# Kernel optimization log

Measured on AMD Instinct MI355X. Metric: run time of the kernel, lower is better.

The kernel has to match this reference:

```python
import jax, jax.numpy as jnp
import numpy as np

DIM = 512
HEADS = 8
EPS = 1e-5


def layer_norm(x, g, b):
    mu = jnp.mean(x, axis=-1, keepdims=True)
    var = jnp.mean(jnp.square(x - mu), axis=-1, keepdims=True)
    return (x - mu) * jax.lax.rsqrt(var + EPS) * g + b


def setup_inputs() -> dict:
    key = jax.random.key(0)
    ks = jax.random.split(key, 8)
    d = DIM
    s = 0.02
    return {
        "x": jax.random.normal(ks[0], (2, d, 64, 64), jnp.float32),
        "ln1_g": jnp.ones((d,), jnp.float32),
        "ln1_b": jnp.zeros((d,), jnp.float32),
        "w_qkv": jax.random.normal(ks[1], (d, 3 * d), jnp.float32) * s,
        "b_qkv": jnp.zeros((3 * d,), jnp.float32),
        "w_proj": jax.random.normal(ks[2], (d, d), jnp.float32) * s,
        "b_proj": jnp.zeros((d,), jnp.float32),
        "ln2_g": jnp.ones((d,), jnp.float32),
        "ln2_b": jnp.zeros((d,), jnp.float32),
        "w_ffn1": jax.random.normal(ks[3], (d, 4 * d), jnp.float32) * s,
        "b_ffn1": jnp.zeros((4 * d,), jnp.float32),
        "w_ffn2": jax.random.normal(ks[4], (4 * d, d), jnp.float32) * s,
        "b_ffn2": jnp.zeros((d,), jnp.float32),
    }


def reference(x, ln1_g, ln1_b, w_qkv, b_qkv, w_proj, b_proj,
              ln2_g, ln2_b, w_ffn1, b_ffn1, w_ffn2, b_ffn2):
    B, C, H, W = x.shape
    hd = C // HEADS
    x_in = x
    t = x.reshape(B, C, H * W).transpose(0, 2, 1)  # [B, N, C]
    h = layer_norm(t, ln1_g, ln1_b)
    qkv = h @ w_qkv + b_qkv  # [B, N, 3C]
    q, k, v = jnp.split(qkv, 3, axis=-1)
    def to_heads(a):
        return a.reshape(B, -1, HEADS, hd).transpose(0, 2, 1, 3)  # [B, h, N, hd]
    q, k, v = to_heads(q), to_heads(k), to_heads(v)
    # NOTE: module scales by 1/sqrt(C), not 1/sqrt(head_dim)
    attn = jnp.einsum('bhqd,bhkd->bhqk', q, k) / jnp.sqrt(jnp.float32(C))
    attn = jax.nn.softmax(attn, axis=-1)
    out = jnp.einsum('bhqk,bhkd->bhqd', attn, v)
    out = out.transpose(0, 2, 1, 3).reshape(B, -1, C)
    out = out @ w_proj + b_proj
    t = t + out
    h2 = layer_norm(t, ln2_g, ln2_b)
    ffn = jax.nn.relu(h2 @ w_ffn1 + b_ffn1) @ w_ffn2 + b_ffn2
    t = t + ffn
    y = t.transpose(0, 2, 1).reshape(B, C, H, W)
    return y + x_in
```

## Files before the change

kernel.cpp:

```cpp
#include <hip/hip_runtime.h>
#include <hip/hip_bf16.h>

typedef __bf16 bf16;
typedef __bf16 bf16x8 __attribute__((ext_vector_type(8)));
typedef __bf16 bf16x4 __attribute__((ext_vector_type(4)));
typedef __bf16 bf16x2 __attribute__((ext_vector_type(2)));
typedef float f32x4 __attribute__((ext_vector_type(4)));
typedef int int4v __attribute__((ext_vector_type(4)));
typedef int int2v __attribute__((ext_vector_type(2)));

#define DEV static __device__ __forceinline__

DEV void gload16(const void* g, void* l) {
    __builtin_amdgcn_global_load_lds(
        (const __attribute__((address_space(1))) void*)g,
        (__attribute__((address_space(3))) void*)l, 16, 0, 0);
}

DEV f32x4 mfma16(bf16x8 a, bf16x8 b, f32x4 c) {
    return __builtin_amdgcn_mfma_f32_16x16x32_bf16(a, b, c, 0, 0, 0);
}

DEV int cvtpk(float lo, float hi) {
    int r;
    asm("v_cvt_pk_bf16_f32 %0, %1, %2" : "=v"(r) : "v"(lo), "v"(hi));
    return r;
}

DEV float rexp2(float x) {
    float r;
    asm("v_exp_f32 %0, %1" : "=v"(r) : "v"(x));
    return r;
}

__global__ __launch_bounds__(512, 2)
void k_pre(const float* __restrict__ x, const float* __restrict__ gg,
           const float* __restrict__ bb, bf16* __restrict__ h,
           const float* __restrict__ w0, const float* __restrict__ w1,
           const float* __restrict__ w2, const float* __restrict__ w3,
           bf16* __restrict__ d0, bf16* __restrict__ d1,
           bf16* __restrict__ d2, bf16* __restrict__ d3) {
    __shared__ char sm[35840];
    int bid = blockIdx.x;
    int t = threadIdx.x;

    if (bid >= 256) {
        float* tile = (float*)sm;
        int tt = bid - 256;
        const float* w;
        bf16* d;
        int K, N, ti;
        if (tt < 768)       { w = w0; d = d0; K = 512;  N = 1536; ti = tt; }
        else if (tt < 1024) { w = w1; d = d1; K = 512;  N = 512;  ti = tt - 768; }
        else if (tt < 2048) { w = w2; d = d2; K = 512;  N = 2048; ti = tt - 1024; }
        else                { w = w3; d = d3; K = 2048; N = 512;  ti = tt - 2048; }
        int ntn = N >> 5;
        int kt = ti / ntn, ntile = ti % ntn;
        int k0 = kt * 32, n0 = ntile * 32;
        int nl = t & 31, kl = t >> 5;
#pragma unroll
        for (int i = 0; i < 2; i++) {
            int k = kl + i * 16;
            tile[k * 33 + nl] = w[(size_t)(k0 + k) * N + n0 + nl];
        }
        __syncthreads();
        int kl2 = t & 31, nl2 = t >> 5;
#pragma unroll
        for (int i = 0; i < 2; i++) {
            int n = nl2 + i * 16;
            d[(size_t)(n0 + n) * K + k0 + kl2] = (bf16)tile[kl2 * 33 + n];
        }
        return;
    }

    bf16* big = (bf16*)sm;
    float* red = (float*)(sm + 33536);
    float* mures = (float*)(sm + 35584);
    int nt = bid & 127, b = bid >> 7;
    int n0 = nt * 32;

    int n = t & 31, cg = t >> 5;
    const float* xp = x + (size_t)b * 512 * 4096 +
                      (size_t)(cg * 32) * 4096 + n0 + n;
    float s = 0.f, ss = 0.f;
#pragma unroll
    for (int i = 0; i < 32; i++) {
        float v = xp[(size_t)i * 4096];
        s += v;
        ss += v * v;
        big[n * 524 + cg * 32 + i] = (bf16)v;
    }
    s += __shfl_xor(s, 32);
    ss += __shfl_xor(ss, 32);
    int w = t >> 6, l = t & 63;
    if (l < 32) {
        red[(w * 32 + n) * 2] = s;
        red[(w * 32 + n) * 2 + 1] = ss;
    }
    __syncthreads();
    if (t < 32) {
        float ts = 0.f, tss = 0.f;
#pragma unroll
        for (int ww = 0; ww < 8; ww++) {
            ts += red[(ww * 32 + t) * 2];
            tss += red[(ww * 32 + t) * 2 + 1];
        }
        float mu = ts * (1.f / 512.f);
        float var = tss * (1.f / 512.f) - mu * mu;
        mures[t * 2] = mu;
        mures[t * 2 + 1] = rsqrtf(var + 1e-5f);
    }
    __syncthreads();

    int nw = t >> 4, cs = t & 15;
    float mu = mures[nw * 2], rs = mures[nw * 2 + 1];
    bf16* hd = h + (size_t)(b * 4096 + n0 + nw) * 512;
#pragma unroll
    for (int j = 0; j < 4; j++) {
        int c = cs * 8 + j * 128;
        bf16x8 vv = *(const bf16x8*)&big[nw * 524 + c];
        f32x4 g0v = *(const f32x4*)(gg + c);
        f32x4 g1v = *(const f32x4*)(gg + c + 4);
        f32x4 b0v = *(const f32x4*)(bb + c);
        f32x4 b1v = *(const f32x4*)(bb + c + 4);
        bf16x8 o;
#pragma unroll
        for (int k = 0; k < 4; k++) {
            o[k] = (bf16)(((float)vv[k] - mu) * rs * g0v[k] + b0v[k]);
            o[k + 4] = (bf16)(((float)vv[k + 4] - mu) * rs * g1v[k] + b1v[k]);
        }
        *(bf16x8*)(hd + c) = o;
    }
}

__global__ __launch_bounds__(512, 2)
void k_tln2(const float* __restrict__ x, const bf16* __restrict__ po,
            const float* __restrict__ gg, const float* __restrict__ bb,
            bf16* __restrict__ h) {
    __shared__ char sm[69632];
    bf16* big = (bf16*)sm;
    float* red = (float*)(sm + 33536);
    float* mures = (float*)(sm + 35584);
    bf16* pob = (bf16*)(sm + 35840);

    int t = threadIdx.x;
    int bid = blockIdx.x;
    int nt = bid & 127, b = bid >> 7;
    int n0 = nt * 32;

    {
        int rr = t >> 4, cs16 = t & 15;
        const bf16* ps = po + (size_t)(b * 4096 + n0 + rr) * 512 + cs16 * 32;
#pragma unroll
        for (int j = 0; j < 4; j++)
            *(bf16x8*)&pob[rr * 524 + cs16 * 32 + j * 8] =
                *(const bf16x8*)(ps + j * 8);
        __syncthreads();
    }

    int n = t & 31, cg = t >> 5;
    const float* xp = x + (size_t)b * 512 * 4096 +
                      (size_t)(cg * 32) * 4096 + n0 + n;
    float s = 0.f, ss = 0.f;
#pragma unroll
    for (int i = 0; i < 32; i++) {
        float v = xp[(size_t)i * 4096] + (float)pob[n * 524 + cg * 32 + i];
        s += v;
        ss += v * v;
        big[n * 524 + cg * 32 + i] = (bf16)v;
    }
    s += __shfl_xor(s, 32);
    ss += __shfl_xor(ss, 32);
    int w = t >> 6, l = t & 63;
    if (l < 32) {
        red[(w * 32 + n) * 2] = s;
        red[(w * 32 + n) * 2 + 1] = ss;
    }
    __syncthreads();
    if (t < 32) {
        float ts = 0.f, tss = 0.f;
#pragma unroll
        for (int ww = 0; ww < 8; ww++) {
            ts += red[(ww * 32 + t) * 2];
            tss += red[(ww * 32 + t) * 2 + 1];
        }
        float mu = ts * (1.f / 512.f);
        float var = tss * (1.f / 512.f) - mu * mu;
        mures[t * 2] = mu;
        mures[t * 2 + 1] = rsqrtf(var + 1e-5f);
    }
    __syncthreads();

    int nw = t >> 4, cs = t & 15;
    float mu = mures[nw * 2], rs = mures[nw * 2 + 1];
    bf16* hd = h + (size_t)(b * 4096 + n0 + nw) * 512;
#pragma unroll
    for (int j = 0; j < 4; j++) {
        int c = cs * 8 + j * 128;
        bf16x8 vv = *(const bf16x8*)&big[nw * 524 + c];
        f32x4 g0v = *(const f32x4*)(gg + c);
        f32x4 g1v = *(const f32x4*)(gg + c + 4);
        f32x4 b0v = *(const f32x4*)(bb + c);
        f32x4 b1v = *(const f32x4*)(bb + c + 4);
        bf16x8 o;
#pragma unroll
        for (int k = 0; k < 4; k++) {
            o[k] = (bf16)(((float)vv[k] - mu) * rs * g0v[k] + b0v[k]);
            o[k + 4] = (bf16)(((float)vv[k + 4] - mu) * rs * g1v[k] + b1v[k]);
        }
        *(bf16x8*)(hd + c) = o;
    }
}

template <int MODE, int BN>
__global__ __launch_bounds__(256, BN == 64 ? 3 : 2)
void k_gemm(const bf16* __restrict__ A, const bf16* __restrict__ BT,
            const float* __restrict__ bias, bf16* __restrict__ outb,
            bf16* __restrict__ vtout, const float* __restrict__ xin,
            const bf16* __restrict__ poin, float* __restrict__ yout,
            int M, int N, int K) {
    constexpr int CG = BN / 32;
    constexpr int BSZ = CG * 4096;
    __shared__ char smem[32768 + 2 * BSZ];
    int ntn = N / BN;
    int nwg = gridDim.x;
    int bid = blockIdx.x;
    int cpx = nwg >> 3;
    bid = (bid & 7) * cpx + (bid >> 3);
    int bm = bid / ntn, bn = bid % ntn;
    int m0 = bm * 128, n0 = bn * BN;
    int tid = threadIdx.x;
    int w = tid >> 6, l = tid & 63;
    int wm = w >> 1, wn = w & 1;
    int l15 = l & 15, lg = l >> 4;

    f32x4 acc[4][CG];
#pragma unroll
    for (int i = 0; i < 4; i++)
#pragma unroll
        for (int j = 0; j < CG; j++) acc[i][j] = (f32x4){0.f, 0.f, 0.f, 0.f};

    int srow = tid >> 3, sphys = tid & 7;
    int lrow_a = wm * 64 + l15;
    int lrow_b = wn * (BN / 2) + l15;

#define GEMM_STAGE(k0v, bb)                                                  \
    do {                                                                     \
        _Pragma("unroll") for (int s = 0; s < 4; s++) {                      \
            int row = s * 32 + srow;                                         \
            int k16 = sphys ^ (row & 7);                                     \
            gload16(A + (size_t)(m0 + row) * K + (k0v) + k16 * 8,            \
                    smem + (bb) * 16384 + s * 4096 + tid * 16);              \
        }                                                                    \
        _Pragma("unroll") for (int s = 0; s < CG; s++) {                     \
            int row = s * 32 + srow;                                         \
            int k16 = sphys ^ (row & 7);                                     \
            gload16(BT + (size_t)(n0 + row) * K + (k0v) + k16 * 8,           \
                    smem + 32768 + (bb) * BSZ + s * 4096 + tid * 16);        \
        }                                                                    \
    } while (0)

    int nk = K >> 6;
    GEMM_STAGE(0, 0);
    int cur = 0;
    for (int kt = 0; kt < nk; kt++) {
        if (kt + 1 < nk) {
            GEMM_STAGE((kt + 1) << 6, cur ^ 1);
            if constexpr (BN == 128)
                asm volatile("s_waitcnt vmcnt(8)" ::: "memory");
            else
                asm volatile("s_waitcnt vmcnt(6)" ::: "memory");
        } else {
            asm volatile("s_waitcnt vmcnt(0)" ::: "memory");
        }
        __builtin_amdgcn_s_barrier();
        __builtin_amdgcn_sched_barrier(0);
        const char* pA = smem + cur * 16384;
        const char* pB = smem + 32768 + cur * BSZ;
#pragma unroll
        for (int ks = 0; ks < 2; ks++) {
            bf16x8 af[4], bfr[CG];
#pragma unroll
            for (int rg = 0; rg < 4; rg++) {
                int row = lrow_a + rg * 16;
                af[rg] = *(const bf16x8*)(pA + row * 128 +
                                          (((lg + ks * 4) ^ (row & 7)) << 4));
            }
#pragma unroll
            for (int cg = 0; cg < CG; cg++) {
                int row = lrow_b + cg * 16;
                bfr[cg] = *(const bf16x8*)(pB + row * 128 +
                                           (((lg + ks * 4) ^ (row & 7)) << 4));
            }
#pragma unroll
            for (int rg = 0; rg < 4; rg++)
#pragma unroll
                for (int cg = 0; cg < CG; cg++)
                    acc[rg][cg] = mfma16(af[rg], bfr[cg], acc[rg][cg]);
        }
        __builtin_amdgcn_s_barrier();
        cur ^= 1;
    }
#undef GEMM_STAGE

    if constexpr (MODE == 2) {
        if (n0 >= 1024) {
            char* vl = smem;
#pragma unroll
            for (int cg = 0; cg < CG; cg++) {
                int col = wn * (BN / 2) + cg * 16 + l15;
                float bz = bias[n0 + col];
#pragma unroll
                for (int rg = 0; rg < 4; rg++) {
                    int rowb = wm * 64 + rg * 16 + lg * 4;
                    int2v qq = {cvtpk(acc[rg][cg][0] + bz, acc[rg][cg][1] + bz),
                                cvtpk(acc[rg][cg][2] + bz, acc[rg][cg][3] + bz)};
                    *(int2v*)(vl + col * 272 + rowb * 2) = qq;
                }
            }
            __syncthreads();
            int b = m0 >> 12, nrow0 = m0 & 4095;
            int dl = tid >> 3, c8 = tid & 7;
#pragma unroll
            for (int dd = 0; dd < BN / 32; dd++) {
                int d = dd * 32 + dl;
                int ch = (n0 - 1024) + d;
                bf16* dst = vtout +
                    ((size_t)((b * 8 + (ch >> 6)) * 64 + (ch & 63))) * 4096 + nrow0;
#pragma unroll
                for (int half = 0; half < 2; half++) {
                    int chunk = half * 8 + c8;
                    bf16x8 vv = *(const bf16x8*)(vl + d * 272 + chunk * 16);
                    *(bf16x8*)(dst + chunk * 8) = vv;
                }
            }
            return;
        }
    }

    if constexpr (MODE == 3) {
        float* ts = (float*)smem;
        int b = m0 >> 12, nrow0 = m0 & 4095;
#pragma unroll
        for (int cg = 0; cg < CG; cg++) {
            int lcol = wn * (BN / 2) + cg * 16 + l15;
            float bz = bias[n0 + lcol];
#pragma unroll
            for (int rg = 0; rg < 4; rg++) {
#pragma unroll
                for (int j = 0; j < 4; j++) {
                    int lrow = wm * 64 + rg * 16 + lg * 4 + j;
                    float v = acc[rg][cg][j] + bz +
                        (float)poin[(size_t)(m0 + lrow) * 512 + n0 + lcol];
                    ts[lcol * 132 + lrow] = v;
                }
            }
        }
        __syncthreads();
        int nl = (tid & 31) * 4, chh = tid >> 5;
#pragma unroll
        for (int q = 0; q < 8; q++) {
            int c = chh + q * 8;
            size_t off = ((size_t)b * 512 + n0 + c) * 4096 + nrow0 + nl;
            f32x4 xv = *(const f32x4*)(xin + off);
            f32x4 tv = *(const f32x4*)&ts[c * 132 + nl];
            f32x4 ov;
#pragma unroll
            for (int k2 = 0; k2 < 4; k2++) ov[k2] = 2.f * xv[k2] + tv[k2];
            *(f32x4*)(yout + off) = ov;
        }
        return;
    }

    constexpr int RS = BN * 2 + 8;
    constexpr int CH = BN / 8;
    char* ep = smem;
#pragma unroll
    for (int cg = 0; cg < CG; cg++) {
        int lcol = wn * (BN / 2) + cg * 16 + l15;
        float bz = bias[n0 + lcol];
#pragma unroll
        for (int rg = 0; rg < 4; rg++) {
#pragma unroll
            for (int j = 0; j < 4; j++) {
                int lrow = wm * 64 + rg * 16 + lg * 4 + j;
                float v = acc[rg][cg][j] + bz;
                *(bf16*)(ep + lrow * RS + lcol * 2) = (bf16)v;
            }
        }
    }
    __syncthreads();
    int cch = tid & (CH - 1);
    int rof = tid / CH;
    constexpr int RPP = 256 / CH;
#pragma unroll
    for (int i = 0; i < 128 / RPP; i++) {
        int row = i * RPP + rof;
        bf16x8 vv = *(const bf16x8*)(ep + row * RS + cch * 16);
        *(bf16x8*)(outb + (size_t)(m0 + row) * N + n0 + cch * 8) = vv;
    }
}

__global__ __launch_bounds__(512, 2)
void k_gemm8(const bf16* __restrict__ A, const bf16* __restrict__ BT,
             const float* __restrict__ bias, bf16* __restrict__ outb) {
    __shared__ char sL[131072];
    int bid = blockIdx.x;
    bid = (bid & 7) * 32 + (bid >> 3);
    int bm = bid >> 3, bn = bid & 7;
    int m0 = bm * 256, n0 = bn * 256;
    int tid = threadIdx.x;
    int w = tid >> 6, l = tid & 63;
    int wm = w >> 2, wn = w & 3;
    int l15 = l & 15, lg = l >> 4;
    int cpr = (lg ^ ((l15 >> 1) & 3)) << 4;

    f32x4 acc[8][4];
#pragma unroll
    for (int i = 0; i < 8; i++)
#pragma unroll
        for (int j = 0; j < 4; j++) acc[i][j] = (f32x4){0.f, 0.f, 0.f, 0.f};

    int srow = tid >> 2, scp = tid & 3;
    int kofs = (scp ^ ((srow >> 1) & 3)) * 8;
    const bf16* gA0 = A + (size_t)(m0 + srow) * 512 + kofs;
    const bf16* gA1 = gA0 + 128 * 512;
    const bf16* gB0 = BT + (size_t)(n0 + srow) * 512 + kofs;
    const bf16* gB1 = gB0 + 128 * 512;
    char* dA = sL + tid * 16;
    char* dB = sL + 65536 + tid * 16;
    const char* pA0 = sL + (wm * 128 + l15) * 64 + cpr;
    const char* pB0 = sL + 65536 + (wn * 64 + l15) * 64 + cpr;

#define STGA(T, S, BUF)                                                       \
    gload16(gA0 + (T) * 64 + (S) * 32, dA + (BUF) * 32768 + (S) * 16384);     \
    gload16(gA1 + (T) * 64 + (S) * 32, dA + (BUF) * 32768 + (S) * 16384 + 8192);
#define STGB(T, S, BUF)                                                       \
    gload16(gB0 + (T) * 64 + (S) * 32, dB + (BUF) * 32768 + (S) * 16384);     \
    gload16(gB1 + (T) * 64 + (S) * 32, dB + (BUF) * 32768 + (S) * 16384 + 8192);
#define WB8 asm volatile("s_waitcnt vmcnt(8)" ::: "memory"); __builtin_amdgcn_s_barrier();
#define WB4 asm volatile("s_waitcnt vmcnt(4)" ::: "memory"); __builtin_amdgcn_s_barrier();
#define WB0 asm volatile("s_waitcnt vmcnt(0)" ::: "memory"); __builtin_amdgcn_s_barrier();
#define WBN

    bf16x8 bfr[4];

#define PH(BUF, S, RGH, WAITC, STGC)                                          \
    {                                                                         \
        WAITC                                                                 \
        if ((RGH) == 0) {                                                     \
            _Pragma("unroll") for (int cg = 0; cg < 4; cg++)                  \
                bfr[cg] = *(const bf16x8*)(pB0 + (BUF) * 32768 +              \
                                           (S) * 16384 + cg * 1024);          \
        }                                                                     \
        bf16x8 af[4];                                                         \
        _Pragma("unroll") for (int i = 0; i < 4; i++)                         \
            af[i] = *(const bf16x8*)(pA0 + (BUF) * 32768 + (S) * 16384 +      \
                                     ((RGH) * 4 + i) * 1024);                 \
        STGC                                                                  \
        __builtin_amdgcn_s_barrier();                                         \
        asm volatile("s_waitcnt lgkmcnt(0)" ::: "memory");                    \
        __builtin_amdgcn_sched_barrier(0);                                    \
        __builtin_amdgcn_s_setprio(1);                                        \
        _Pragma("unroll") for (int i = 0; i < 4; i++)                         \
            _Pragma("unroll") for (int cg = 0; cg < 4; cg++)                  \
                acc[(RGH) * 4 + i][cg] =                                      \
                    mfma16(af[i], bfr[cg], acc[(RGH) * 4 + i][cg]);           \
        __builtin_amdgcn_s_setprio(0);                                        \
    }

#define TILEF(T, BUF)                                                         \
    PH(BUF, 0, 0, WB8, STGA(T + 1, 1, BUF ^ 1))                               \
    PH(BUF, 0, 1, WBN, STGB(T + 1, 1, BUF ^ 1))                               \
    PH(BUF, 1, 0, WB8, STGA(T + 2, 0, BUF))                                   \
    PH(BUF, 1, 1, WBN, STGB(T + 2, 0, BUF))

    STGA(0, 0, 0) STGB(0, 0, 0) STGA(0, 1, 0) STGB(0, 1, 0)
    STGA(1, 0, 1) STGB(1, 0, 1)

    TILEF(0, 0) TILEF(1, 1) TILEF(2, 0) TILEF(3, 1) TILEF(4, 0) TILEF(5, 1)
    PH(0, 0, 0, WB8, STGA(7, 1, 1))
    PH(0, 0, 1, WBN, STGB(7, 1, 1))
    PH(0, 1, 0, WB8, )
    PH(0, 1, 1, WBN, )
    PH(1, 0, 0, WB4, )
    PH(1, 0, 1, WBN, )
    PH(1, 1, 0, WB0, )
    PH(1, 1, 1, WBN, )
#undef TILEF
#undef PH
#undef WB8
#undef WB4
#undef WB0
#undef WBN
#undef STGA
#undef STGB

    float bz[4];
#pragma unroll
    for (int cg = 0; cg < 4; cg++) bz[cg] = bias[n0 + wn * 64 + cg * 16 + l15];
#pragma unroll
    for (int h2 = 0; h2 < 2; h2++) {
        __syncthreads();
        if (wm == h2) {
#pragma unroll
            for (int rg = 0; rg < 8; rg++)
#pragma unroll
                for (int cg = 0; cg < 4; cg++)
#pragma unroll
                    for (int j = 0; j < 4; j++) {
                        int rl = rg * 16 + lg * 4 + j;
                        int cl = wn * 64 + cg * 16 + l15;
                        float v = fmaxf(acc[rg][cg][j] + bz[cg], 0.f);
                        *(bf16*)(sL + rl * 520 + cl * 2) = (bf16)v;
                    }
        }
        __syncthreads();
        int cch = tid & 31, rof = tid >> 5;
#pragma unroll
        for (int p = 0; p < 8; p++) {
            int row = p * 16 + rof;
            bf16x8 vv = *(const bf16x8*)(sL + row * 520 + cch * 16);
            *(bf16x8*)(outb + (size_t)(m0 + h2 * 128 + row) * 2048 +
                       n0 + cch * 8) = vv;
        }
    }
}

__global__ __launch_bounds__(512, 4)
void k_attn(const bf16* __restrict__ qkvb, const bf16* __restrict__ vt,
            bf16* __restrict__ attno) {
    __shared__ bf16 sK[2][64 * 64];
    __shared__ bf16 sV[2][64 * 64];
    const float sc = 0.044194173824159216f * 1.4426950408889634f;
    int bid = blockIdx.x;
    int nb = (bid & 7) * 64 + (bid >> 3);
    int bh = nb >> 5, qt = nb & 31;
    int b = bh >> 3, hh = bh & 7;
    int q0 = qt * 128;
    int tid = threadIdx.x, w = tid >> 6, l = tid & 63;
    int l15 = l & 15, lg = l >> 4, l7 = l15 & 7;
    int vperm = ((lg & 1) << 1) | (lg >> 1);
    const bf16* qbase = qkvb + (size_t)b * 4096 * 1536 + hh * 64;
    const bf16* kbase = qbase + 512;
    const bf16* vbase = vt + (size_t)bh * 64 * 4096;
    int srow = tid >> 3, sphys = tid & 7;

    const char* kp0 = (const char*)&sK[0][0] + l15 * 128 + ((lg ^ l7) << 4);
    const char* kp1 = (const char*)&sK[0][0] + l15 * 128 + (((4 + lg) ^ l7) << 4);
    const char* vp0 = (const char*)&sV[0][0] + l15 * 128 + ((vperm ^ l7) << 4);
    const char* vp1 = (const char*)&sV[0][0] + l15 * 128 + (((4 + vperm) ^ l7) << 4);
    char* dK0 = (char*)&sK[0][0] + tid * 16;
    char* dV0 = (char*)&sV[0][0] + tid * 16;
    const char* kg = (const char*)(kbase + srow * 1536 + (sphys ^ (srow & 7)) * 8);
    const char* vg = (const char*)(vbase + srow * 4096 + (sphys ^ (srow & 7)) * 8);

    gload16(kg, dK0);
    gload16(vg, dV0);
    kg += 196608;
    vg += 128;

    bf16x8 qf[2];
#pragma unroll
    for (int ks = 0; ks < 2; ks++) {
        bf16x8 v = *(const bf16x8*)(qbase +
            (size_t)(q0 + w * 16 + l15) * 1536 + ks * 32 + lg * 8);
        bf16x8 o;
#pragma unroll
        for (int j = 0; j < 8; j++) o[j] = (bf16)((float)v[j] * sc);
        qf[ks] = o;
    }
    bf16x8 ones;
#pragma unroll
    for (int j = 0; j < 8; j++) ones[j] = (bf16)1.0f;

    const f32x4 kZ = {0.f, 0.f, 0.f, 0.f};
    f32x4 accl = kZ;
    f32x4 acc[4];
#pragma unroll
    for (int df = 0; df < 4; df++) acc[df] = kZ;

#define ABODY(BUF, PF)                                                        \
    {                                                                         \
        if (PF) {                                                             \
            gload16(kg, dK0 + (1 - (BUF)) * 8192);                            \
            gload16(vg, dV0 + (1 - (BUF)) * 8192);                            \
            kg += 196608;                                                     \
            vg += 128;                                                        \
            asm volatile("s_waitcnt vmcnt(2)" ::: "memory");                  \
        } else {                                                              \
            asm volatile("s_waitcnt vmcnt(0)" ::: "memory");                  \
        }                                                                     \
        __builtin_amdgcn_s_barrier();                                         \
        __builtin_amdgcn_sched_barrier(0);                                    \
        f32x4 s0, s1, s2, s3;                                                 \
        __builtin_amdgcn_s_setprio(1);                                        \
        s0 = mfma16(*(const bf16x8*)(kp0 + (BUF) * 8192 + 0 * 2048), qf[0], kZ); \
        s0 = mfma16(*(const bf16x8*)(kp1 + (BUF) * 8192 + 0 * 2048), qf[1], s0); \
        s1 = mfma16(*(const bf16x8*)(kp0 + (BUF) * 8192 + 1 * 2048), qf[0], kZ); \
        s1 = mfma16(*(const bf16x8*)(kp1 + (BUF) * 8192 + 1 * 2048), qf[1], s1); \
        __builtin_amdgcn_s_setprio(0);                                        \
        float e0 = rexp2(s0[0]), e1 = rexp2(s0[1]);                           \
        float e2 = rexp2(s0[2]), e3 = rexp2(s0[3]);                           \
        float e4 = rexp2(s1[0]), e5 = rexp2(s1[1]);                           \
        float e6 = rexp2(s1[2]), e7 = rexp2(s1[3]);                           \
        __builtin_amdgcn_s_setprio(1);                                        \
        s2 = mfma16(*(const bf16x8*)(kp0 + (BUF) * 8192 + 2 * 2048), qf[0], kZ); \
        s2 = mfma16(*(const bf16x8*)(kp1 + (BUF) * 8192 + 2 * 2048), qf[1], s2); \
        s3 = mfma16(*(const bf16x8*)(kp0 + (BUF) * 8192 + 3 * 2048), qf[0], kZ); \
        s3 = mfma16(*(const bf16x8*)(kp1 + (BUF) * 8192 + 3 * 2048), qf[1], s3); \
        __builtin_amdgcn_s_setprio(0);                                        \
        int p0 = cvtpk(e0, e1), p1 = cvtpk(e2, e3);                           \
        int p2 = cvtpk(e4, e5), p3 = cvtpk(e6, e7);                           \
        asm("v_permlane16_swap_b32 %0, %1" : "+v"(p2), "+v"(p0));             \
        asm("v_permlane16_swap_b32 %0, %1" : "+v"(p3), "+v"(p1));             \
        {                                                                     \
            int4v ai = {p0, p1, p2, p3};                                      \
            bf16x8 af = __builtin_bit_cast(bf16x8, ai);                       \
            __builtin_amdgcn_s_setprio(1);                                    \
            acc[0] = mfma16(af, *(const bf16x8*)(vp0 + (BUF) * 8192 + 0 * 2048), acc[0]); \
            acc[1] = mfma16(af, *(const bf16x8*)(vp0 + (BUF) * 8192 + 1 * 2048), acc[1]); \
            acc[2] = mfma16(af, *(const bf16x8*)(vp0 + (BUF) * 8192 + 2 * 2048), acc[2]); \
            acc[3] = mfma16(af, *(const bf16x8*)(vp0 + (BUF) * 8192 + 3 * 2048), acc[3]); \
            accl = mfma16(af, ones, accl);                                    \
            __builtin_amdgcn_s_setprio(0);                                    \
        }                                                                     \
        float e8 = rexp2(s2[0]), e9 = rexp2(s2[1]);                           \
        float e10 = rexp2(s2[2]), e11 = rexp2(s2[3]);                         \
        float e12 = rexp2(s3[0]), e13 = rexp2(s3[1]);                         \
        float e14 = rexp2(s3[2]), e15 = rexp2(s3[3]);                         \
        int p4 = cvtpk(e8, e9), p5 = cvtpk(e10, e11);                         \
        int p6 = cvtpk(e12, e13), p7 = cvtpk(e14, e15);                       \
        asm("v_permlane16_swap_b32 %0, %1" : "+v"(p6), "+v"(p4));             \
        asm("v_permlane16_swap_b32 %0, %1" : "+v"(p7), "+v"(p5));             \
        {                                                                     \
            int4v ai = {p4, p5, p6, p7};                                      \
            bf16x8 af = __builtin_bit_cast(bf16x8, ai);                       \
            __builtin_amdgcn_s_setprio(1);                                    \
            acc[0] = mfma16(af, *(const bf16x8*)(vp1 + (BUF) * 8192 + 0 * 2048), acc[0]); \
            acc[1] = mfma16(af, *(const bf16x8*)(vp1 + (BUF) * 8192 + 1 * 2048), acc[1]); \
            acc[2] = mfma16(af, *(const bf16x8*)(vp1 + (BUF) * 8192 + 2 * 2048), acc[2]); \
            acc[3] = mfma16(af, *(const bf16x8*)(vp1 + (BUF) * 8192 + 3 * 2048), acc[3]); \
            accl = mfma16(af, ones, accl);                                    \
            __builtin_amdgcn_s_setprio(0);                                    \
        }                                                                     \
        __builtin_amdgcn_s_barrier();                                         \
    }

    for (int tt = 0; tt < 31; tt++) {
        ABODY(0, 1)
        ABODY(1, 1)
    }
    ABODY(0, 1)
    ABODY(1, 0)
#undef ABODY

    float invq[4];
#pragma unroll
    for (int j = 0; j < 4; j++) invq[j] = 1.0f / accl[j];

    bf16* ow = (bf16*)&sK[0][0] + w * 16 * 64;
#pragma unroll
    for (int df = 0; df < 4; df++) {
        int chunk = df * 2 + (l15 >> 3);
        int within = l15 & 7;
#pragma unroll
        for (int j = 0; j < 4; j++) {
            int q = lg * 4 + j;
            *(bf16*)((char*)ow + q * 128 + ((chunk ^ (q & 7)) << 4) + within * 2) =
                (bf16)(acc[df][j] * invq[j]);
        }
    }
    __syncthreads();
    const char* owr = (const char*)ow;
#pragma unroll
    for (int half = 0; half < 2; half++) {
        int r = l >> 2, ch = (l & 3) + half * 4;
        bf16x8 vv = *(const bf16x8*)(owr + r * 128 + ((ch ^ (r & 7)) << 4));
        *(bf16x8*)(attno + (size_t)(b * 4096 + q0 + w * 16 + r) * 512 +
                   hh * 64 + ch * 8) = vv;
    }
}

extern "C" void kernel_launch(void* const* d_in, const int* in_sizes, int n_in,
                              void* d_out, int out_size, void* d_ws, size_t ws_size,
                              hipStream_t stream) {
    const float* x = (const float*)d_in[0];
    const float* ln1g = (const float*)d_in[1];
    const float* ln1b = (const float*)d_in[2];
    const float* wqkv = (const float*)d_in[3];
    const float* bqkv = (const float*)d_in[4];
    const float* wproj = (const float*)d_in[5];
    const float* bproj = (const float*)d_in[6];
    const float* ln2g = (const float*)d_in[7];
    const float* ln2b = (const float*)d_in[8];
    const float* wffn1 = (const float*)d_in[9];
    const float* bffn1 = (const float*)d_in[10];
    const float* wffn2 = (const float*)d_in[11];
    const float* bffn2 = (const float*)d_in[12];
    float* y = (float*)d_out;

    char* ws = (char*)d_ws;
    bf16* po   = (bf16*)(ws + 0);
    bf16* h    = (bf16*)(ws + 16777216);
    bf16* qkvb = (bf16*)(ws + 25165824);
    bf16* vtb  = (bf16*)(ws + 50331648);
    bf16* f1   = (bf16*)(ws + 25165824);
    bf16* wqT  = (bf16*)(ws + 58720256);
    bf16* wpT  = (bf16*)(ws + 60293120);
    bf16* w1T  = (bf16*)(ws + 60817408);
    bf16* w2T  = (bf16*)(ws + 62914560);
    bf16* attno = h;

    k_pre<<<3328, 512, 0, stream>>>(x, ln1g, ln1b, h,
                                    wqkv, wproj, wffn1, wffn2,
                                    wqT, wpT, w1T, w2T);
    k_gemm<2, 128><<<768, 256, 0, stream>>>(h, wqT, bqkv, qkvb, vtb,
                                            nullptr, nullptr, nullptr,
                                            8192, 1536, 512);
    k_attn<<<512, 512, 0, stream>>>(qkvb, vtb, attno);
    k_gemm<0, 64><<<512, 256, 0, stream>>>(attno, wpT, bproj, po, nullptr,
                                           nullptr, nullptr, nullptr,
                                           8192, 512, 512);
    k_tln2<<<256, 512, 0, stream>>>(x, po, ln2g, ln2b, h);
    k_gemm8<<<256, 512, 0, stream>>>(h, w1T, bffn1, f1);
    k_gemm<3, 64><<<512, 256, 0, stream>>>(f1, w2T, bffn2, nullptr, nullptr,
                                           x, po, y, 8192, 512, 2048);
}
```

Before: 172.0 us.

## Split attention KV range across two blocks and add a combine kernel

Each attention block now processes half of the key/value sequence, which doubles the grid to 1024 blocks. Each block writes an unnormalized partial output and its partial row sums to workspace buffers that reuse the po and wqT regions. A new k_comb kernel adds the two partials and divides by the summed denominators; this works without a max correction because the softmax uses no running-max subtraction. The aim is better CU occupancy and load balance, paid for with extra global traffic for the partials, one more launch, and a higher launch_bounds occupancy target that may force register spills.

```diff
diff --git a/kernel.cpp b/kernel.cpp
--- a/kernel.cpp
+++ b/kernel.cpp
@@ -527,14 +527,15 @@
     }
 }
 
-__global__ __launch_bounds__(512, 4)
+__global__ __launch_bounds__(512, 8)
 void k_attn(const bf16* __restrict__ qkvb, const bf16* __restrict__ vt,
-            bf16* __restrict__ attno) {
+            bf16* __restrict__ part, float* __restrict__ lpart) {
     __shared__ bf16 sK[2][64 * 64];
     __shared__ bf16 sV[2][64 * 64];
     const float sc = 0.044194173824159216f * 1.4426950408889634f;
     int bid = blockIdx.x;
-    int nb = (bid & 7) * 64 + (bid >> 3);
+    int nb2 = (bid & 7) * 128 + (bid >> 3);
+    int nb = nb2 >> 1, half = nb2 & 1;
     int bh = nb >> 5, qt = nb & 31;
     int b = bh >> 3, hh = bh & 7;
     int q0 = qt * 128;
@@ -552,8 +553,10 @@
     const char* vp1 = (const char*)&sV[0][0] + l15 * 128 + (((4 + vperm) ^ l7) << 4);
     char* dK0 = (char*)&sK[0][0] + tid * 16;
     char* dV0 = (char*)&sV[0][0] + tid * 16;
-    const char* kg = (const char*)(kbase + srow * 1536 + (sphys ^ (srow & 7)) * 8);
-    const char* vg = (const char*)(vbase + srow * 4096 + (sphys ^ (srow & 7)) * 8);
+    const char* kg = (const char*)(kbase +
+        (size_t)(half * 2048 + srow) * 1536 + (sphys ^ (srow & 7)) * 8);
+    const char* vg = (const char*)(vbase + (size_t)srow * 4096 +
+        half * 2048 + (sphys ^ (srow & 7)) * 8);
 
     gload16(kg, dK0);
     gload16(vg, dV0);
@@ -647,7 +650,7 @@
         __builtin_amdgcn_s_barrier();                                         \
     }
 
-    for (int tt = 0; tt < 31; tt++) {
+    for (int tt = 0; tt < 15; tt++) {
         ABODY(0, 1)
         ABODY(1, 1)
     }
@@ -655,10 +658,6 @@
     ABODY(1, 0)
 #undef ABODY
 
-    float invq[4];
-#pragma unroll
-    for (int j = 0; j < 4; j++) invq[j] = 1.0f / accl[j];
-
     bf16* ow = (bf16*)&sK[0][0] + w * 16 * 64;
 #pragma unroll
     for (int df = 0; df < 4; df++) {
@@ -668,17 +667,48 @@
         for (int j = 0; j < 4; j++) {
             int q = lg * 4 + j;
             *(bf16*)((char*)ow + q * 128 + ((chunk ^ (q & 7)) << 4) + within * 2) =
-                (bf16)(acc[df][j] * invq[j]);
-        }
+                (bf16)acc[df][j];
+        }
+    }
+    if (l15 == 0) {
+#pragma unroll
+        for (int j = 0; j < 4; j++)
+            lpart[(size_t)nb2 * 128 + w * 16 + lg * 4 + j] = accl[j];
     }
     __syncthreads();
     const char* owr = (const char*)ow;
-#pragma unroll
-    for (int half = 0; half < 2; half++) {
-        int r = l >> 2, ch = (l & 3) + half * 4;
+    bf16* pdst = part + (size_t)nb2 * 8192 + w * 16 * 64;
+#pragma unroll
+    for (int hf = 0; hf < 2; hf++) {
+        int r = l >> 2, ch = (l & 3) + hf * 4;
         bf16x8 vv = *(const bf16x8*)(owr + r * 128 + ((ch ^ (r & 7)) << 4));
-        *(bf16x8*)(attno + (size_t)(b * 4096 + q0 + w * 16 + r) * 512 +
-                   hh * 64 + ch * 8) = vv;
+        *(bf16x8*)(pdst + r * 64 + ch * 8) = vv;
+    }
+}
+
+__global__ __launch_bounds__(256)
+void k_comb(const bf16* __restrict__ part, const float* __restrict__ lpart,
+            bf16* __restrict__ attno) {
+    int nb = blockIdx.x;
+    int bh = nb >> 5, qt = nb & 31;
+    int b = bh >> 3, hh = bh & 7;
+    int q0 = qt * 128;
+    int tid = threadIdx.x;
+    int r = tid >> 1, dh = (tid & 1) * 32;
+    const bf16* p0 = part + (size_t)nb * 2 * 8192 + r * 64 + dh;
+    const bf16* p1 = p0 + 8192;
+    float inv = 1.0f / (lpart[(size_t)nb * 256 + r] +
+                        lpart[(size_t)nb * 256 + 128 + r]);
+    bf16* dst = attno + (size_t)(b * 4096 + q0 + r) * 512 + hh * 64 + dh;
+#pragma unroll
+    for (int c4 = 0; c4 < 4; c4++) {
+        bf16x8 a = *(const bf16x8*)(p0 + c4 * 8);
+        bf16x8 bb8 = *(const bf16x8*)(p1 + c4 * 8);
+        bf16x8 o;
+#pragma unroll
+        for (int j = 0; j < 8; j++)
+            o[j] = (bf16)(((float)a[j] + (float)bb8[j]) * inv);
+        *(bf16x8*)(dst + c4 * 8) = o;
     }
 }
 
@@ -701,15 +731,17 @@
     float* y = (float*)d_out;
 
     char* ws = (char*)d_ws;
-    bf16* po   = (bf16*)(ws + 0);
-    bf16* h    = (bf16*)(ws + 16777216);
-    bf16* qkvb = (bf16*)(ws + 25165824);
-    bf16* vtb  = (bf16*)(ws + 50331648);
-    bf16* f1   = (bf16*)(ws + 25165824);
-    bf16* wqT  = (bf16*)(ws + 58720256);
-    bf16* wpT  = (bf16*)(ws + 60293120);
-    bf16* w1T  = (bf16*)(ws + 60817408);
-    bf16* w2T  = (bf16*)(ws + 62914560);
+    bf16* po    = (bf16*)(ws + 0);
+    bf16* part  = (bf16*)(ws + 0);
+    bf16* h     = (bf16*)(ws + 16777216);
+    bf16* qkvb  = (bf16*)(ws + 25165824);
+    bf16* vtb   = (bf16*)(ws + 50331648);
+    bf16* f1    = (bf16*)(ws + 25165824);
+    bf16* wqT   = (bf16*)(ws + 58720256);
+    float* lpart = (float*)(ws + 58720256);
+    bf16* wpT   = (bf16*)(ws + 60293120);
+    bf16* w1T   = (bf16*)(ws + 60817408);
+    bf16* w2T   = (bf16*)(ws + 62914560);
     bf16* attno = h;
 
     k_pre<<<3328, 512, 0, stream>>>(x, ln1g, ln1b, h,
@@ -718,7 +750,8 @@
     k_gemm<2, 128><<<768, 256, 0, stream>>>(h, wqT, bqkv, qkvb, vtb,
                                             nullptr, nullptr, nullptr,
                                             8192, 1536, 512);
-    k_attn<<<512, 512, 0, stream>>>(qkvb, vtb, attno);
+    k_attn<<<1024, 512, 0, stream>>>(qkvb, vtb, part, lpart);
+    k_comb<<<512, 256, 0, stream>>>(part, lpart, attno);
     k_gemm<0, 64><<<512, 256, 0, stream>>>(attno, wpT, bproj, po, nullptr,
                                            nullptr, nullptr, nullptr,
                                            8192, 512, 512);
```

New measurement: 180.0 us. 4.6% more time.
